# Kernel tuning notes

Measured on AMD Instinct MI355X. Metric: run time of the kernel, lower is better.

The kernel has to match this reference:

```python
import jax, jax.numpy as jnp
import numpy as np

B, N, E, D_IN, D_OUT = 16, 2048, 65536, 256, 256


def setup_inputs() -> dict:
    key = jax.random.key(0)
    k1, k2, k3 = jax.random.split(key, 3)
    node_features = jax.random.normal(k1, (B, N, D_IN), dtype=jnp.float32)
    edge_indices = jax.random.randint(k2, (B, 2, E), 0, N, dtype=jnp.int64)
    W = jax.random.normal(k3, (D_OUT, 2 * D_IN), dtype=jnp.float32) * (1.0 / np.sqrt(2 * D_IN))
    b = jnp.zeros((D_OUT,), dtype=jnp.float32)
    return {"node_features": node_features, "edge_indices": edge_indices, "W": W, "b": b}


def reference(node_features, edge_indices, W, b):
    # node_features: [B, N, D]; edge_indices: [B, 2, E] (src row 0, dst row 1)
    n_nodes = node_features.shape[1]
    src = edge_indices[:, 0, :]  # [B, E]
    dst = edge_indices[:, 1, :]  # [B, E]
    # gather source-node features per edge: [B, E, D]
    gathered = jnp.take_along_axis(node_features, src[:, :, None], axis=1)

    def per_graph(feats_g, dst_g):
        s = jax.ops.segment_sum(feats_g, dst_g, num_segments=n_nodes)          # [N, D]
        c = jax.ops.segment_sum(jnp.ones_like(dst_g, dtype=feats_g.dtype),
                                dst_g, num_segments=n_nodes)                    # [N]
        return s / jnp.maximum(c, 1.0)[:, None]  # mean; 0 for isolated nodes

    neighbor_agg = jax.vmap(per_graph)(gathered, dst)            # [B, N, D]
    combined = jnp.concatenate([node_features, neighbor_agg], axis=-1)  # [B, N, 2D]
    return jnp.einsum('bnd,od->bno', combined, W) + b
```

## Files before the change

kernel.cpp:

```cpp
#include <hip/hip_runtime.h>
#include <hip/hip_bf16.h>

#define BATCH 16
#define NNODE 2048
#define NEDGE 65536
#define DIN   256
#define DOUT  256
#define KDIM  512
#define SUB   16
#define ESUB  (NEDGE/SUB)

typedef __attribute__((ext_vector_type(8))) short short8;
typedef __attribute__((ext_vector_type(4))) float f32x4;

__device__ __forceinline__ ushort f2bf(float f) {
    union { float f; unsigned u; } v; v.f = f;
    unsigned u = v.u;
    unsigned r = (u + 0x7fffu + ((u >> 16) & 1u)) >> 16;
    return (ushort)r;
}

__device__ __forceinline__ int q8(float x) {
    float c = fminf(fmaxf(x * 16.0f, -127.0f), 127.0f);
    return (int)rintf(c);
}

__device__ __forceinline__ unsigned f2e4m3(float x) {
    unsigned u = __float_as_uint(x);
    unsigned s = (u >> 24) & 0x80u;
    float ax = __uint_as_float(u & 0x7FFFFFFFu);
    if (ax >= 448.0f) return s | 0x7Eu;
    if (ax < 0.0009765625f) return s;
    if (ax < 0.015625f) {
        int q = (int)rintf(ax * 512.0f);
        return s | (unsigned)q;
    }
    unsigned au = __float_as_uint(ax);
    int e = (int)((au >> 23) & 0xFF) - 127;
    unsigned m = au & 0x7FFFFFu;
    unsigned keep = m >> 20;
    unsigned rest = m & 0xFFFFFu;
    keep += (rest > 0x80000u) || (rest == 0x80000u && (keep & 1u));
    unsigned val = ((unsigned)(e + 7) << 3) + keep;
    if (val > 0x7Eu) val = 0x7Eu;
    return s | val;
}
template <bool HI>
__device__ __forceinline__ unsigned pk2_fp8(float a, float b, unsigned old) {
#if __has_builtin(__builtin_amdgcn_cvt_pk_fp8_f32)
    return (unsigned)__builtin_amdgcn_cvt_pk_fp8_f32(a, b, (int)old, HI);
#else
    unsigned p = f2e4m3(a) | (f2e4m3(b) << 8);
    return HI ? ((old & 0xFFFFu) | (p << 16)) : ((old & 0xFFFF0000u) | p);
#endif
}

#define ASYNC_COPY16(gsrc, ldst) \
    __builtin_amdgcn_global_load_lds((const __attribute__((address_space(1))) void*)(gsrc), \
                                     (__attribute__((address_space(3))) void*)(ldst), 16, 0, 0)

__global__ __launch_bounds__(256) void prep_kernel(
        const float* __restrict__ X, const float* __restrict__ W,
        const int* __restrict__ E,
        int* __restrict__ partial,
        ushort* __restrict__ Xbf, unsigned char* __restrict__ Xi8,
        ushort* __restrict__ Wbf, unsigned char* __restrict__ Wf8s) {
    int bid = blockIdx.x;
    int t = threadIdx.x;
    if (bid < 256) {
        __shared__ int hist[NNODE];
        int b = bid & 15, sub = bid >> 4;
#pragma unroll
        for (int j = 0; j < 8; ++j) hist[t + j * 256] = 0;
        __syncthreads();
        const int4* dsts = reinterpret_cast<const int4*>(
            E + (size_t)b * 2 * NEDGE + NEDGE + sub * ESUB);
#pragma unroll
        for (int j = 0; j < 4; ++j) {
            int4 d = dsts[j * 256 + t];
            atomicAdd(&hist[d.x], 1);
            atomicAdd(&hist[d.y], 1);
            atomicAdd(&hist[d.z], 1);
            atomicAdd(&hist[d.w], 1);
        }
        __syncthreads();
        int* pb = partial + ((size_t)b * SUB + sub) * NNODE;
#pragma unroll
        for (int j = 0; j < 8; ++j) pb[t + j * 256] = hist[t + j * 256];
    } else if (bid < 4352) {
        size_t i = (size_t)(bid - 256) * 256 + t;
        const float4* p = reinterpret_cast<const float4*>(X + i * 8);
        float4 u = p[0], v = p[1];
        ushort4 o0 = { f2bf(u.x), f2bf(u.y), f2bf(u.z), f2bf(u.w) };
        ushort4 o1 = { f2bf(v.x), f2bf(v.y), f2bf(v.z), f2bf(v.w) };
        *reinterpret_cast<ushort4*>(Xbf + i * 8)     = o0;
        *reinterpret_cast<ushort4*>(Xbf + i * 8 + 4) = o1;
        unsigned q0 = (q8(u.x) & 255) | ((q8(u.y) & 255) << 8) |
                      ((q8(u.z) & 255) << 16) | ((unsigned)(q8(u.w) & 255) << 24);
        unsigned q1 = (q8(v.x) & 255) | ((q8(v.y) & 255) << 8) |
                      ((q8(v.z) & 255) << 16) | ((unsigned)(q8(v.w) & 255) << 24);
        uint2 q = { q0, q1 };
        *reinterpret_cast<uint2*>(Xi8 + i * 8) = q;
    } else {
        int i = (bid - 4352) * 256 + t;
        int col = i >> 6;
        int k = (i & 63) * 8;
        const float4* p = reinterpret_cast<const float4*>(W + (size_t)col * KDIM + k);
        float4 u = p[0], v = p[1];
        if (k < DIN) {
            ushort4 o0 = { f2bf(u.x), f2bf(u.y), f2bf(u.z), f2bf(u.w) };
            ushort4 o1 = { f2bf(v.x), f2bf(v.y), f2bf(v.z), f2bf(v.w) };
            *reinterpret_cast<ushort4*>(Wbf + (size_t)col * KDIM + k)     = o0;
            *reinterpret_cast<ushort4*>(Wbf + (size_t)col * KDIM + k + 4) = o1;
        } else {
            unsigned w0 = pk2_fp8<false>(u.x, u.y, 0u);
            w0 = pk2_fp8<true>(u.z, u.w, w0);
            unsigned w1 = pk2_fp8<false>(v.x, v.y, 0u);
            w1 = pk2_fp8<true>(v.z, v.w, w1);
            int kk = k - DIN;
            int kt = kk >> 5, kq = (kk >> 3) & 3;
            uint2 qv = { w0, w1 };
            *reinterpret_cast<uint2*>(Wf8s + (size_t)kt * 8192 + kq * 2048 + col * 8) = qv;
        }
    }
}

__global__ __launch_bounds__(256) void fillscan_kernel(
        const int* __restrict__ E,
        const int* __restrict__ partial,
        int* __restrict__ counts, int* __restrict__ cursor,
        int* __restrict__ srcIdx) {
    __shared__ int cur[NNODE];
    __shared__ int tsum[256];
    int bid = blockIdx.x;
    int t = threadIdx.x;
    int b = bid & 15, sub = bid >> 4;
    const int* pb = partial + (size_t)b * SUB * NNODE;

    int tot[8] = {}, pre[8] = {};
    for (int k = 0; k < SUB; ++k) {
        const int4* p = reinterpret_cast<const int4*>(pb + k * NNODE + t * 8);
        int4 a = p[0], c = p[1];
        if (k < sub) {
            pre[0] += a.x; pre[1] += a.y; pre[2] += a.z; pre[3] += a.w;
            pre[4] += c.x; pre[5] += c.y; pre[6] += c.z; pre[7] += c.w;
        }
        tot[0] += a.x; tot[1] += a.y; tot[2] += a.z; tot[3] += a.w;
        tot[4] += c.x; tot[5] += c.y; tot[6] += c.z; tot[7] += c.w;
    }
    int s = 0;
#pragma unroll
    for (int j = 0; j < 8; ++j) s += tot[j];
    tsum[t] = s;
    __syncthreads();
    for (int off = 1; off < 256; off <<= 1) {
        int v = (t >= off) ? tsum[t - off] : 0;
        __syncthreads();
        tsum[t] += v;
        __syncthreads();
    }
    int run = (t == 0) ? 0 : tsum[t - 1];
    bool writer = (sub == 0);
    int base = b * NNODE + t * 8;
#pragma unroll
    for (int j = 0; j < 8; ++j) {
        cur[t * 8 + j] = run + pre[j];
        if (writer) { counts[base + j] = tot[j]; cursor[base + j] = run; }
        run += tot[j];
    }
    __syncthreads();

    const int* eb = E + (size_t)b * 2 * NEDGE;
    const int4* srcs = reinterpret_cast<const int4*>(eb + sub * ESUB);
    const int4* dsts = reinterpret_cast<const int4*>(eb + NEDGE + sub * ESUB);
    int* sb = srcIdx + (size_t)b * NEDGE;
#pragma unroll
    for (int j = 0; j < 4; ++j) {
        int4 sv = srcs[j * 256 + t];
        int4 dv = dsts[j * 256 + t];
        sb[atomicAdd(&cur[dv.x], 1)] = sv.x;
        sb[atomicAdd(&cur[dv.y], 1)] = sv.y;
        sb[atomicAdd(&cur[dv.z], 1)] = sv.z;
        sb[atomicAdd(&cur[dv.w], 1)] = sv.w;
    }
}

__global__ __launch_bounds__(256) void aggregate_kernel(
        const unsigned char* __restrict__ Xi8,
        const int* __restrict__ srcIdx,
        const int* __restrict__ cursor,
        const int* __restrict__ counts,
        unsigned char* __restrict__ Gq) {
    int bid = blockIdx.x;
    int blk = (bid & 7) * 1024 + (bid >> 3);
    int wave = threadIdx.x >> 6;
    int lane = threadIdx.x & 63;
    int q = lane >> 4;
    int l16 = lane & 15;
    int f0 = l16 * 16;
    int node = blk * 4 + wave;
    int b = node >> 11;
    int deg = counts[node];
    int start = cursor[node];
    const unsigned char* xb = Xi8 + (size_t)b * NNODE * DIN;
    const int* sidx = srcIdx + (size_t)b * NEDGE + start;

    unsigned a0 = 0, a1 = 0, a2 = 0, a3 = 0, a4 = 0, a5 = 0, a6 = 0, a7 = 0;
#define M16 0x00FF00FFu
#define ACC16(v) do {                                                         \
        unsigned w0 = (v).x ^ 0x80808080u, w1 = (v).y ^ 0x80808080u;          \
        unsigned w2 = (v).z ^ 0x80808080u, w3 = (v).w ^ 0x80808080u;          \
        a0 += w0 & M16;  a1 += (w0 >> 8) & M16;                               \
        a2 += w1 & M16;  a3 += (w1 >> 8) & M16;                               \
        a4 += w2 & M16;  a5 += (w2 >> 8) & M16;                               \
        a6 += w3 & M16;  a7 += (w3 >> 8) & M16;                               \
    } while (0)

    int i = 0;
    for (; i + 16 <= deg; i += 16) {
        int s0 = sidx[i + q], s1 = sidx[i + 4 + q];
        int s2 = sidx[i + 8 + q], s3 = sidx[i + 12 + q];
        uint4 v0 = *reinterpret_cast<const uint4*>(xb + (size_t)s0 * DIN + f0);
        uint4 v1 = *reinterpret_cast<const uint4*>(xb + (size_t)s1 * DIN + f0);
        uint4 v2 = *reinterpret_cast<const uint4*>(xb + (size_t)s2 * DIN + f0);
        uint4 v3 = *reinterpret_cast<const uint4*>(xb + (size_t)s3 * DIN + f0);
        ACC16(v0); ACC16(v1); ACC16(v2); ACC16(v3);
    }
    for (; i < deg; i += 4) {
        int e = i + q;
        uint4 v = { 0x80808080u, 0x80808080u, 0x80808080u, 0x80808080u };
        if (e < deg)
            v = *reinterpret_cast<const uint4*>(xb + (size_t)sidx[e] * DIN + f0);
        ACC16(v);
    }
#undef ACC16
#undef M16
    a0 += (unsigned)__shfl_xor((int)a0, 16, 64); a0 += (unsigned)__shfl_xor((int)a0, 32, 64);
    a1 += (unsigned)__shfl_xor((int)a1, 16, 64); a1 += (unsigned)__shfl_xor((int)a1, 32, 64);
    a2 += (unsigned)__shfl_xor((int)a2, 16, 64); a2 += (unsigned)__shfl_xor((int)a2, 32, 64);
    a3 += (unsigned)__shfl_xor((int)a3, 16, 64); a3 += (unsigned)__shfl_xor((int)a3, 32, 64);
    a4 += (unsigned)__shfl_xor((int)a4, 16, 64); a4 += (unsigned)__shfl_xor((int)a4, 32, 64);
    a5 += (unsigned)__shfl_xor((int)a5, 16, 64); a5 += (unsigned)__shfl_xor((int)a5, 32, 64);
    a6 += (unsigned)__shfl_xor((int)a6, 16, 64); a6 += (unsigned)__shfl_xor((int)a6, 32, 64);
    a7 += (unsigned)__shfl_xor((int)a7, 16, 64); a7 += (unsigned)__shfl_xor((int)a7, 32, 64);

    if (q == 0) {
        float sc = 1.0f / (16.0f * (float)max(deg, 1));
        float bs = 128.0f * (float)deg;
        float f[16];
        f[ 0] = ((float)(int)(a0 & 0xFFFFu) - bs) * sc;
        f[ 2] = ((float)(int)(a0 >> 16)     - bs) * sc;
        f[ 1] = ((float)(int)(a1 & 0xFFFFu) - bs) * sc;
        f[ 3] = ((float)(int)(a1 >> 16)     - bs) * sc;
        f[ 4] = ((float)(int)(a2 & 0xFFFFu) - bs) * sc;
        f[ 6] = ((float)(int)(a2 >> 16)     - bs) * sc;
        f[ 5] = ((float)(int)(a3 & 0xFFFFu) - bs) * sc;
        f[ 7] = ((float)(int)(a3 >> 16)     - bs) * sc;
        f[ 8] = ((float)(int)(a4 & 0xFFFFu) - bs) * sc;
        f[10] = ((float)(int)(a4 >> 16)     - bs) * sc;
        f[ 9] = ((float)(int)(a5 & 0xFFFFu) - bs) * sc;
        f[11] = ((float)(int)(a5 >> 16)     - bs) * sc;
        f[12] = ((float)(int)(a6 & 0xFFFFu) - bs) * sc;
        f[14] = ((float)(int)(a6 >> 16)     - bs) * sc;
        f[13] = ((float)(int)(a7 & 0xFFFFu) - bs) * sc;
        f[15] = ((float)(int)(a7 >> 16)     - bs) * sc;
        unsigned wds[4];
#pragma unroll
        for (int w = 0; w < 4; ++w) {
            unsigned t0 = pk2_fp8<false>(f[4 * w], f[4 * w + 1], 0u);
            wds[w] = pk2_fp8<true>(f[4 * w + 2], f[4 * w + 3], t0);
        }
        int panel = node >> 7, r = node & 127;
        int slot = l16 ^ ((r >> 1) & 7);
        uint4 val;
        if (r & 1) { val.x = wds[2]; val.y = wds[3]; val.z = wds[0]; val.w = wds[1]; }
        else       { val.x = wds[0]; val.y = wds[1]; val.z = wds[2]; val.w = wds[3]; }
        *reinterpret_cast<uint4*>(
            Gq + ((size_t)panel * 2048 + r * 16 + slot) * 16) = val;
    }
}

__global__ __launch_bounds__(256) void gemm_kernel(
        const ushort* __restrict__ Xbf,
        const unsigned char* __restrict__ Gq,
        const ushort* __restrict__ Wbf,
        const unsigned char* __restrict__ Wf8s,
        const float* __restrict__ bias,
        float* __restrict__ out) {
    __shared__ ushort As[2][128 * 32];
    __shared__ ushort Bs[2][128 * 32];
    __shared__ uint4  GqV[2048];

    const int tid = threadIdx.x;
    const int wid = tid >> 6, lane = tid & 63;

    int orig = blockIdx.x;
    int logical = (orig & 7) * 64 + (orig >> 3);
    int bx = logical >> 1;
    int by = logical & 1;
    const int rowBase = bx * 128;
    const int colBase = by * 128;
    const int wm = wid >> 1, wn = wid & 1;

    f32x4 acc[4][4] = {};

    const int lk = (((lane & 3) ^ ((lane >> 3) & 3)) * 8);
    const ushort* Arow = Xbf + (size_t)rowBase * DIN;
    const ushort* Brow = Wbf + (size_t)colBase * KDIM;
    const unsigned char* GqPanel = Gq + (size_t)bx * 32768;
    const int r0 = wid * 16 + (lane >> 2);

#define STAGE_X(k0, buf) do {                                                 \
        ASYNC_COPY16(Arow + (size_t)r0 * DIN + (k0) + lk,         &As[buf][wid * 512]);       \
        ASYNC_COPY16(Arow + (size_t)(r0 + 64) * DIN + (k0) + lk,  &As[buf][2048 + wid * 512]);\
        ASYNC_COPY16(Brow + (size_t)r0 * KDIM + (k0) + lk,        &Bs[buf][wid * 512]);       \
        ASYNC_COPY16(Brow + (size_t)(r0 + 64) * KDIM + (k0) + lk, &Bs[buf][2048 + wid * 512]);\
    } while (0)
#define GQ_STAGE(t8) \
        ASYNC_COPY16(GqPanel + (t8) * 4096 + wid * 1024 + lane * 16, \
                     (char*)GqV + (t8) * 4096 + wid * 1024)
#define SG8_STAGE(kt) \
        ASYNC_COPY16(Wf8s + (size_t)(kt) * 8192 + wid * 2048 + ((size_t)colBase + lane * 2) * 8, \
                     (char*)&Bs[(kt) & 1][0] + wid * 1024)

    const int fl = lane & 15;
    const int kq = lane >> 4;
    const int fc = (kq ^ ((fl >> 1) & 3)) * 8;
    const long* GqL = reinterpret_cast<const long*>(GqV);

    STAGE_X(0, 0);
    for (int t = 0; t < 16; ++t) {
        if (t < 7) {
            GQ_STAGE(t);
            STAGE_X((t + 1) * 32, (t + 1) & 1);
            asm volatile("s_waitcnt vmcnt(5)" ::: "memory");
        } else if (t == 7) {
            GQ_STAGE(7);
            SG8_STAGE(0);
            asm volatile("s_waitcnt vmcnt(2)" ::: "memory");
        } else if (t < 15) {
            SG8_STAGE(t - 7);
            asm volatile("s_waitcnt vmcnt(1)" ::: "memory");
        } else {
            asm volatile("s_waitcnt vmcnt(0)" ::: "memory");
        }
        __builtin_amdgcn_s_barrier();

        if (t < 8) {
            const int bufx = t & 1;
            short8 a[4], bb[4];
#pragma unroll
            for (int m = 0; m < 4; ++m)
                a[m] = *reinterpret_cast<const short8*>(
                    &As[bufx][(wm * 64 + m * 16 + fl) * 32 + fc]);
#pragma unroll
            for (int n = 0; n < 4; ++n)
                bb[n] = *reinterpret_cast<const short8*>(
                    &Bs[bufx][(wn * 64 + n * 16 + fl) * 32 + fc]);
#pragma unroll
            for (int m = 0; m < 4; ++m)
#pragma unroll
                for (int n = 0; n < 4; ++n)
                    acc[m][n] = __builtin_amdgcn_mfma_f32_16x16x32_bf16(
                        a[m], bb[n], acc[m][n], 0, 0, 0);
        } else {
            const int kt = t - 8;
            const unsigned char* Bf8 =
                reinterpret_cast<const unsigned char*>(&Bs[kt & 1][0]);
            long ag[4], bg[4];
#pragma unroll
            for (int m = 0; m < 4; ++m) {
                int r = wm * 64 + m * 16 + fl;
                ag[m] = GqL[r * 32 + ((kt * 4 + kq) ^ (r & 15))];
            }
#pragma unroll
            for (int n = 0; n < 4; ++n) {
                int c = wn * 64 + n * 16 + fl;
                bg[n] = *reinterpret_cast<const long*>(Bf8 + kq * 1024 + c * 8);
            }
#pragma unroll
            for (int m = 0; m < 4; ++m)
#pragma unroll
                for (int n = 0; n < 4; ++n)
                    acc[m][n] = __builtin_amdgcn_mfma_f32_16x16x32_fp8_fp8(
                        ag[m], bg[n], acc[m][n], 0, 0, 0);
        }
        __builtin_amdgcn_s_barrier();
    }
#undef STAGE_X
#undef GQ_STAGE
#undef SG8_STAGE

    const int cl = lane & 15, rq = lane >> 4;
#pragma unroll
    for (int n = 0; n < 4; ++n) {
        int col = colBase + wn * 64 + n * 16 + cl;
        float bv = bias[col];
#pragma unroll
        for (int m = 0; m < 4; ++m) {
            int r0o = rowBase + wm * 64 + m * 16 + rq * 4;
#pragma unroll
            for (int j = 0; j < 4; ++j)
                out[(size_t)(r0o + j) * DOUT + col] = acc[m][n][j] + bv;
        }
    }
}

extern "C" void kernel_launch(void* const* d_in, const int* in_sizes, int n_in,
                              void* d_out, int out_size, void* d_ws, size_t ws_size,
                              hipStream_t stream) {
    const float* X    = (const float*)d_in[0];
    const int*   E    = (const int*)d_in[1];
    const float* W    = (const float*)d_in[2];
    const float* bias = (const float*)d_in[3];
    float* out = (float*)d_out;

    char* ws = (char*)d_ws;
    ushort* Xbf  = (ushort*)ws;
    unsigned char* Xi8 = (unsigned char*)(Xbf + (size_t)BATCH * NNODE * DIN);
    ushort* Wbf  = (ushort*)(Xi8 + (size_t)BATCH * NNODE * DIN);
    unsigned char* Wf8s = (unsigned char*)(Wbf + (size_t)DOUT * KDIM);
    int* counts  = (int*)(Wf8s + 8 * 8192);
    int* cursor  = counts + BATCH * NNODE;
    int* srcIdx  = cursor + BATCH * NNODE;
    int* partial = srcIdx + (size_t)BATCH * NEDGE;
    unsigned char* Gq = (unsigned char*)(partial + (size_t)BATCH * SUB * NNODE);

    prep_kernel<<<4416, 256, 0, stream>>>(X, W, E, partial, Xbf, Xi8, Wbf, Wf8s);

    fillscan_kernel<<<256, 256, 0, stream>>>(E, partial, counts, cursor, srcIdx);

    aggregate_kernel<<<(BATCH * NNODE) / 4, 256, 0, stream>>>(
        Xi8, srcIdx, cursor, counts, Gq);

    dim3 ggrid(512);
    gemm_kernel<<<ggrid, 256, 0, stream>>>(Xbf, Gq, Wbf, Wf8s, bias, out);
}
```

Before: 67.35 us.

## Retile GEMM to 64-row by full 256-column blocks

Changes the GEMM block tile from 128x128 to 64 rows by all 256 output columns, with each wave owning a 64-column strip across all 64 rows. The gathered fp8 aggregate panel is now loaded once per row block instead of twice (once per column half), which removes redundant reads of the X and Gq operands. In exchange each block loads the full W tile every k-step, so W traffic per block doubles, and the async-copy counts and waitcnt thresholds are retuned to match. The grid size stays the same, while the shared-memory layout and the fp8 B swizzle stride change.

New measurement: 69.75 us. +3.6%, slower.

```diff
diff --git a/kernel.cpp b/kernel.cpp
--- a/kernel.cpp
+++ b/kernel.cpp
@@ -287,41 +287,43 @@
         const unsigned char* __restrict__ Wf8s,
         const float* __restrict__ bias,
         float* __restrict__ out) {
-    __shared__ ushort As[2][128 * 32];
-    __shared__ ushort Bs[2][128 * 32];
-    __shared__ uint4  GqV[2048];
+    __shared__ ushort As[2][64 * 32];
+    __shared__ ushort Bs[2][256 * 32];
+    __shared__ uint4  GqV[1024];
 
     const int tid = threadIdx.x;
     const int wid = tid >> 6, lane = tid & 63;
 
     int orig = blockIdx.x;
     int logical = (orig & 7) * 64 + (orig >> 3);
-    int bx = logical >> 1;
-    int by = logical & 1;
-    const int rowBase = bx * 128;
-    const int colBase = by * 128;
-    const int wm = wid >> 1, wn = wid & 1;
+    const int rowBase = logical * 64;
 
     f32x4 acc[4][4] = {};
 
-    const int lk = (((lane & 3) ^ ((lane >> 3) & 3)) * 8);
+    const int sr = tid >> 2;
+    const int lk = (((tid & 3) ^ ((tid >> 3) & 3)) * 8);
     const ushort* Arow = Xbf + (size_t)rowBase * DIN;
-    const ushort* Brow = Wbf + (size_t)colBase * KDIM;
-    const unsigned char* GqPanel = Gq + (size_t)bx * 32768;
-    const int r0 = wid * 16 + (lane >> 2);
-
-#define STAGE_X(k0, buf) do {                                                 \
-        ASYNC_COPY16(Arow + (size_t)r0 * DIN + (k0) + lk,         &As[buf][wid * 512]);       \
-        ASYNC_COPY16(Arow + (size_t)(r0 + 64) * DIN + (k0) + lk,  &As[buf][2048 + wid * 512]);\
-        ASYNC_COPY16(Brow + (size_t)r0 * KDIM + (k0) + lk,        &Bs[buf][wid * 512]);       \
-        ASYNC_COPY16(Brow + (size_t)(r0 + 64) * KDIM + (k0) + lk, &Bs[buf][2048 + wid * 512]);\
+    const unsigned char* GqSlice = Gq + (size_t)(logical >> 1) * 32768
+                                      + (size_t)(logical & 1) * 16384;
+
+#define STAGE_X(k0, buf) do {                                                  \
+        ASYNC_COPY16(Arow + (size_t)sr * DIN + (k0) + lk,                      \
+                     &As[buf][wid * 512]);                                     \
+        _Pragma("unroll")                                                      \
+        for (int p = 0; p < 4; ++p)                                            \
+            ASYNC_COPY16(Wbf + (size_t)(p * 64 + sr) * KDIM + (k0) + lk,       \
+                         &Bs[buf][p * 2048 + wid * 512]);                      \
     } while (0)
-#define GQ_STAGE(t8) \
-        ASYNC_COPY16(GqPanel + (t8) * 4096 + wid * 1024 + lane * 16, \
-                     (char*)GqV + (t8) * 4096 + wid * 1024)
-#define SG8_STAGE(kt) \
-        ASYNC_COPY16(Wf8s + (size_t)(kt) * 8192 + wid * 2048 + ((size_t)colBase + lane * 2) * 8, \
-                     (char*)&Bs[(kt) & 1][0] + wid * 1024)
+#define GQ_STAGE(t4) \
+        ASYNC_COPY16(GqSlice + (t4) * 4096 + wid * 1024 + lane * 16, \
+                     (char*)GqV + (t4) * 4096 + wid * 1024)
+#define SG8_STAGE(kt) do {                                                     \
+        _Pragma("unroll")                                                      \
+        for (int j = 0; j < 2; ++j)                                            \
+            ASYNC_COPY16(Wf8s + (size_t)(kt) * 8192 + wid * 2048 + j * 1024    \
+                             + lane * 16,                                      \
+                         (char*)&Bs[(kt) & 1][0] + wid * 2048 + j * 1024);     \
+    } while (0)
 
     const int fl = lane & 15;
     const int kq = lane >> 4;
@@ -330,17 +332,19 @@
 
     STAGE_X(0, 0);
     for (int t = 0; t < 16; ++t) {
-        if (t < 7) {
+        if (t < 4) {
             GQ_STAGE(t);
+            STAGE_X((t + 1) * 32, (t + 1) & 1);
+            asm volatile("s_waitcnt vmcnt(6)" ::: "memory");
+        } else if (t < 7) {
             STAGE_X((t + 1) * 32, (t + 1) & 1);
             asm volatile("s_waitcnt vmcnt(5)" ::: "memory");
         } else if (t == 7) {
-            GQ_STAGE(7);
             SG8_STAGE(0);
             asm volatile("s_waitcnt vmcnt(2)" ::: "memory");
         } else if (t < 15) {
             SG8_STAGE(t - 7);
-            asm volatile("s_waitcnt vmcnt(1)" ::: "memory");
+            asm volatile("s_waitcnt vmcnt(2)" ::: "memory");
         } else {
             asm volatile("s_waitcnt vmcnt(0)" ::: "memory");
         }
@@ -352,11 +356,11 @@
 #pragma unroll
             for (int m = 0; m < 4; ++m)
                 a[m] = *reinterpret_cast<const short8*>(
-                    &As[bufx][(wm * 64 + m * 16 + fl) * 32 + fc]);
+                    &As[bufx][(m * 16 + fl) * 32 + fc]);
 #pragma unroll
             for (int n = 0; n < 4; ++n)
                 bb[n] = *reinterpret_cast<const short8*>(
-                    &Bs[bufx][(wn * 64 + n * 16 + fl) * 32 + fc]);
+                    &Bs[bufx][(wid * 64 + n * 16 + fl) * 32 + fc]);
 #pragma unroll
             for (int m = 0; m < 4; ++m)
 #pragma unroll
@@ -370,13 +374,13 @@
             long ag[4], bg[4];
 #pragma unroll
             for (int m = 0; m < 4; ++m) {
-                int r = wm * 64 + m * 16 + fl;
+                int r = m * 16 + fl;
                 ag[m] = GqL[r * 32 + ((kt * 4 + kq) ^ (r & 15))];
             }
 #pragma unroll
             for (int n = 0; n < 4; ++n) {
-                int c = wn * 64 + n * 16 + fl;
-                bg[n] = *reinterpret_cast<const long*>(Bf8 + kq * 1024 + c * 8);
+                int c = wid * 64 + n * 16 + fl;
+                bg[n] = *reinterpret_cast<const long*>(Bf8 + kq * 2048 + c * 8);
             }
 #pragma unroll
             for (int m = 0; m < 4; ++m)
@@ -394,11 +398,11 @@
     const int cl = lane & 15, rq = lane >> 4;
 #pragma unroll
     for (int n = 0; n < 4; ++n) {
-        int col = colBase + wn * 64 + n * 16 + cl;
+        int col = wid * 64 + n * 16 + cl;
         float bv = bias[col];
 #pragma unroll
         for (int m = 0; m < 4; ++m) {
-            int r0o = rowBase + wm * 64 + m * 16 + rq * 4;
+            int r0o = rowBase + m * 16 + rq * 4;
 #pragma unroll
             for (int j = 0; j < 4; ++j)
                 out[(size_t)(r0o + j) * DOUT + col] = acc[m][n][j] + bv;
```
